# Kernel tuning notes

Hardware: AMD Instinct MI355X
Metric: run time of the kernel (lower is better)

## Reference

```python
import jax, jax.numpy as jnp
import numpy as np

NUM_SITES = 64
PHYS_DIM = 2
BOND_DIM = 32
BATCH = 65536


def _build_mps(num_sites, phys_dim, bond_dim, seed=0):
    """Replicates ImprovedMPS._initialize_tensors + _canonical_form, then
    zero-pads ragged cores into a dense [S, D, p, D] stack."""
    rng = np.random.default_rng(seed)
    tensors = []
    cur = 1
    for i in range(num_sites):
        if i == 0:
            nb = min(bond_dim, phys_dim)
            shape = (1, phys_dim, nb)
            cur = nb
        elif i == num_sites - 1:
            shape = (cur, phys_dim, 1)
        else:
            nb = min(bond_dim, cur * phys_dim)
            shape = (cur, phys_dim, nb)
            cur = nb
        ld, rd = shape[0] * shape[1], shape[2]
        m = (rng.standard_normal((ld, rd)) * 0.1).astype(np.float32)
        if ld >= rd:
            q, _ = np.linalg.qr(m)
            t = q.reshape(shape)
        else:
            q, _ = np.linalg.qr(m.T)
            t = q.T.reshape(shape)
        tensors.append(t.astype(np.float32))
    # left-canonical sweep
    for i in range(num_sites - 1):
        l, p, r = tensors[i].shape
        q, rr = np.linalg.qr(tensors[i].reshape(l * p, r))
        tensors[i] = q.reshape(l, p, q.shape[1]).astype(np.float32)
        nl, npd, nr = tensors[i + 1].shape
        tensors[i + 1] = (rr @ tensors[i + 1].reshape(nl, npd * nr)).reshape(rr.shape[0], npd, nr).astype(np.float32)
    # zero-pad ragged bonds into dense stack [S, D, p, D]
    A = np.zeros((num_sites, bond_dim, phys_dim, bond_dim), dtype=np.float32)
    for i, t in enumerate(tensors):
        l, p, r = t.shape
        A[i, :l, :, :r] = t
    return A


def setup_inputs() -> dict:
    key = jax.random.key(0)
    x_batch = jax.random.normal(key, (BATCH, NUM_SITES, PHYS_DIM), dtype=jnp.float32)
    A = jnp.asarray(_build_mps(NUM_SITES, PHYS_DIM, BOND_DIM))
    return {"x_batch": x_batch, "A": A}


def reference(x_batch, A):
    # x_batch: [B, S, p]; A: [S, D, p, D] (zero-padded ragged MPS cores)
    B = x_batch.shape[0]
    D = A.shape[1]
    # left_vector starts as ones(B,1) in the ragged view == one-hot e0 in padded view
    left0 = jnp.zeros((B, D), dtype=x_batch.dtype).at[:, 0].set(1.0)
    xs = jnp.moveaxis(x_batch, 1, 0)  # [S, B, p]

    def step(left, inp):
        A_i, x_i = inp  # [D, p, D], [B, p]
        # fuses: contracted = einsum('bp,lpd->bld'); left = einsum('bl,bld->bd')
        left = jnp.einsum('bl,bp,lpd->bd', left, x_i, A_i)
        return left, None

    left, _ = jax.lax.scan(step, left0, (A, xs))
    return left[:, :1]  # last core has right bond 1 -> only col 0 is nonzero
```

## Files before the change

### kernel.cpp

```cpp
#include <hip/hip_runtime.h>


typedef _Float16 half8 __attribute__((ext_vector_type(8)));
typedef float floatx16 __attribute__((ext_vector_type(16)));
typedef float f32x4 __attribute__((ext_vector_type(4)));

#define NPAIRS 32
#define CHUNK_ELEMS 16384

__global__ void mps_prep_pair(const float* __restrict__ A, _Float16* __restrict__ Gf) {
    __shared__ float sA0[2048], sA1[2048], sG[4096];
    const int P = blockIdx.x, tid = threadIdx.x;
    const float* a0p = A + (size_t)(2 * P) * 2048;
    const float* a1p = A + (size_t)(2 * P + 1) * 2048;
#pragma unroll
    for (int i = 0; i < 8; ++i) {
        sA0[tid + 256 * i] = a0p[tid + 256 * i];
        sA1[tid + 256 * i] = a1p[tid + 256 * i];
    }
    __syncthreads();
    {
        const int l = tid >> 3, pq = (tid >> 1) & 3, dh16 = (tid & 1) * 16;
        const int p = pq >> 1, q = pq & 1;
        float accv[16];
#pragma unroll
        for (int dd = 0; dd < 16; ++dd) accv[dd] = 0.f;
        for (int m = 0; m < 32; ++m) {
            const float av = sA0[l * 64 + p * 32 + m];
            const float* bp = &sA1[m * 64 + q * 32 + dh16];
#pragma unroll
            for (int dd = 0; dd < 16; ++dd) accv[dd] += av * bp[dd];
        }
#pragma unroll
        for (int dd = 0; dd < 16; ++dd) sG[l * 128 + pq * 32 + dh16 + dd] = accv[dd];
    }
    __syncthreads();
    const int lane = tid & 63;
    const int h    = lane >> 5;
    const int d    = lane & 31;
#pragma unroll
    for (int pass = 0; pass < 2; ++pass) {
        const int kf = (tid >> 6) + pass * 4;
        const int pq = kf >> 1, lh = kf & 1;
        half8 v;
#pragma unroll
        for (int e = 0; e < 8; ++e) {
            const int l = 16 * lh + (e & 3) + 8 * (e >> 2) + 4 * h;
            v[e] = (_Float16)sG[l * 128 + pq * 32 + d];
        }
        reinterpret_cast<half8*>(Gf)[((size_t)P * 8 + kf) * 64 + lane] = v;
    }
}

#define MF32(A_, B_, C_) __builtin_amdgcn_mfma_f32_32x32x16_f16(A_, B_, C_, 0, 0, 0)

#define PAIR1(G, CIN, COUT, XV)                                               \
    {                                                                         \
        half8 FA0_, FA1_;                                                     \
        _Pragma("unroll")                                                     \
        for (int i_ = 0; i_ < 8; ++i_) {                                      \
            FA0_[i_] = (_Float16)CIN[i_];                                     \
            FA1_[i_] = (_Float16)CIN[8 + i_];                                 \
        }                                                                     \
        const _Float16 w0_ = (_Float16)(XV[0] * XV[2]);                       \
        const _Float16 w1_ = (_Float16)(XV[0] * XV[3]);                       \
        const _Float16 w2_ = (_Float16)(XV[1] * XV[2]);                       \
        const _Float16 w3_ = (_Float16)(XV[1] * XV[3]);                       \
        half8 W0_, W1_, W2_, W3_;                                             \
        _Pragma("unroll")                                                     \
        for (int i_ = 0; i_ < 8; ++i_) {                                      \
            W0_[i_] = w0_; W1_[i_] = w1_; W2_[i_] = w2_; W3_[i_] = w3_;       \
        }                                                                     \
        COUT = MF32(G[0], FA0_ * W0_, zv);                                    \
        COUT = MF32(G[1], FA1_ * W0_, COUT);                                  \
        COUT = MF32(G[2], FA0_ * W1_, COUT);                                  \
        COUT = MF32(G[3], FA1_ * W1_, COUT);                                  \
        COUT = MF32(G[4], FA0_ * W2_, COUT);                                  \
        COUT = MF32(G[5], FA1_ * W2_, COUT);                                  \
        COUT = MF32(G[6], FA0_ * W3_, COUT);                                  \
        COUT = MF32(G[7], FA1_ * W3_, COUT);                                  \
    }

#define RD(DST, BUF, PL)                                                      \
    {                                                                         \
        _Pragma("unroll")                                                     \
        for (int f_ = 0; f_ < 8; ++f_)                                        \
            DST[f_] = *(const half8*)&smA[(BUF) * CHUNK_ELEMS                 \
                                          + (((PL) * 8 + f_) * 64 + lane) * 8]; \
    }

#define STAGE(C, BUF)                                                         \
    {                                                                         \
        _Pragma("unroll")                                                     \
        for (int r_ = 0; r_ < 16; ++r_) {                                     \
            const int rec_ = r_ * 2 + wid;                                    \
            const _Float16* g_ = Gf + (size_t)(C) * CHUNK_ELEMS               \
                                 + rec_ * 512 + lane * 8;                     \
            __builtin_amdgcn_global_load_lds(                                 \
                (const __attribute__((address_space(1))) void*)g_,            \
                (__attribute__((address_space(3))) void*)&smA[(BUF) * CHUNK_ELEMS + rec_ * 512], \
                16, 0, 0);                                                    \
        }                                                                     \
    }

#define CHUNKB(C, BUF, XT0, XT1, XN0, XN1)                                    \
    {                                                                         \
        if ((C) < 7) {                                                        \
            STAGE((C) + 1, 1 - (BUF));                                        \
            _Pragma("unroll")                                                 \
            for (int pp_ = 0; pp_ < 4; ++pp_) {                               \
                XN0[pp_] = xp0[4 * ((C) + 1) + pp_];                          \
                XN1[pp_] = xp1[4 * ((C) + 1) + pp_];                          \
            }                                                                 \
        }                                                                     \
        RD(GB, BUF, 1)                                                        \
        PAIR1(GA, c0, d0, XT0[0])                                             \
        PAIR1(GA, c1, d1, XT1[0])                                             \
        RD(GA, BUF, 2)                                                        \
        PAIR1(GB, d0, c0, XT0[1])                                             \
        PAIR1(GB, d1, c1, XT1[1])                                             \
        RD(GB, BUF, 3)                                                        \
        PAIR1(GA, c0, d0, XT0[2])                                             \
        PAIR1(GA, c1, d1, XT1[2])                                             \
        PAIR1(GB, d0, c0, XT0[3])                                             \
        PAIR1(GB, d1, c1, XT1[3])                                             \
        __syncthreads();                                                      \
        if ((C) < 7) RD(GA, 1 - (BUF), 0)                                     \
    }

__global__ __launch_bounds__(128, 1) void mps_main(const float* __restrict__ x,
                                                   const _Float16* __restrict__ Gf,
                                                   float* __restrict__ out) {
    __shared__ __align__(16) _Float16 smA[2 * CHUNK_ELEMS];

    const int lane  = threadIdx.x & 63;
    const int wid   = threadIdx.x >> 6;
    const int wbase = (blockIdx.x * 2 + wid) * 64;
    const int col   = lane & 31;

    const f32x4* xp0 = reinterpret_cast<const f32x4*>(x + (size_t)(wbase + col) * 128);
    const f32x4* xp1 = reinterpret_cast<const f32x4*>(x + (size_t)(wbase + 32 + col) * 128);

    floatx16 zv;
#pragma unroll
    for (int i = 0; i < 16; ++i) zv[i] = 0.f;

    floatx16 c0, c1, d0, d1;
#pragma unroll
    for (int i = 0; i < 16; ++i) { c0[i] = 0.f; c1[i] = 0.f; d0[i] = 0.f; d1[i] = 0.f; }
    if (lane < 32) { c0[0] = 1.f; c1[0] = 1.f; }

    f32x4 xa0[4], xa1[4], xb0[4], xb1[4];
    half8 GA[8], GB[8];

    STAGE(0, 0);
#pragma unroll
    for (int pp = 0; pp < 4; ++pp) { xa0[pp] = xp0[pp]; xa1[pp] = xp1[pp]; }
    __syncthreads();
    RD(GA, 0, 0)

    CHUNKB(0, 0, xa0, xa1, xb0, xb1)
    CHUNKB(1, 1, xb0, xb1, xa0, xa1)
    CHUNKB(2, 0, xa0, xa1, xb0, xb1)
    CHUNKB(3, 1, xb0, xb1, xa0, xa1)
    CHUNKB(4, 0, xa0, xa1, xb0, xb1)
    CHUNKB(5, 1, xb0, xb1, xa0, xa1)
    CHUNKB(6, 0, xa0, xa1, xb0, xb1)
    CHUNKB(7, 1, xb0, xb1, xa0, xa1)

    if (lane < 32) {
        out[wbase + lane]      = c0[0];
        out[wbase + 32 + lane] = c1[0];
    }
}

extern "C" void kernel_launch(void* const* d_in, const int* in_sizes, int n_in,
                              void* d_out, int out_size, void* d_ws, size_t ws_size,
                              hipStream_t stream) {
    const float* x = (const float*)d_in[0];
    const float* A = (const float*)d_in[1];
    float* outp = (float*)d_out;
    _Float16* Gf = (_Float16*)d_ws;

    hipLaunchKernelGGL(mps_prep_pair, dim3(NPAIRS), dim3(256), 0, stream, A, Gf);
    hipLaunchKernelGGL(mps_main, dim3(65536 / 128), dim3(128), 0, stream, x, Gf, outp);
}
```

Before: 29.24 us.

## Split MFMA accumulation chains and stage x through LDS via async loads

Each pair step now keeps two independent MFMA accumulator chains (even and odd K halves) and sums them when forming the next step's input. This halves the length of the dependent MFMA chain. The x inputs are now prefetched into a double-buffered LDS region with global_load_lds alongside the G staging, replacing per-lane register prefetches. This uses more LDS and adds extra adds and LDS reads per step, in exchange for more MFMA instruction-level parallelism and fewer live registers.

```diff
diff --git a/kernel.cpp b/kernel.cpp
--- a/kernel.cpp
+++ b/kernel.cpp
@@ -6,7 +6,8 @@
 typedef float f32x4 __attribute__((ext_vector_type(4)));
 
 #define NPAIRS 32
-#define CHUNK_ELEMS 16384
+#define GCHUNK 16384
+#define XCHUNK 2048
 
 __global__ void mps_prep_pair(const float* __restrict__ A, _Float16* __restrict__ Gf) {
     __shared__ float sA0[2048], sA1[2048], sG[4096];
@@ -54,76 +55,94 @@
 
 #define MF32(A_, B_, C_) __builtin_amdgcn_mfma_f32_32x32x16_f16(A_, B_, C_, 0, 0, 0)
 
-#define PAIR1(G, CIN, COUT, XV)                                               \
+#define PAIRT(G, AA, AB, XQ)                                                  \
     {                                                                         \
         half8 FA0_, FA1_;                                                     \
         _Pragma("unroll")                                                     \
         for (int i_ = 0; i_ < 8; ++i_) {                                      \
-            FA0_[i_] = (_Float16)CIN[i_];                                     \
-            FA1_[i_] = (_Float16)CIN[8 + i_];                                 \
-        }                                                                     \
-        const _Float16 w0_ = (_Float16)(XV[0] * XV[2]);                       \
-        const _Float16 w1_ = (_Float16)(XV[0] * XV[3]);                       \
-        const _Float16 w2_ = (_Float16)(XV[1] * XV[2]);                       \
-        const _Float16 w3_ = (_Float16)(XV[1] * XV[3]);                       \
+            FA0_[i_] = (_Float16)(AA[i_] + AB[i_]);                           \
+            FA1_[i_] = (_Float16)(AA[8 + i_] + AB[8 + i_]);                   \
+        }                                                                     \
+        const _Float16 w0_ = (_Float16)(XQ[0] * XQ[2]);                       \
+        const _Float16 w1_ = (_Float16)(XQ[0] * XQ[3]);                       \
+        const _Float16 w2_ = (_Float16)(XQ[1] * XQ[2]);                       \
+        const _Float16 w3_ = (_Float16)(XQ[1] * XQ[3]);                       \
         half8 W0_, W1_, W2_, W3_;                                             \
         _Pragma("unroll")                                                     \
         for (int i_ = 0; i_ < 8; ++i_) {                                      \
             W0_[i_] = w0_; W1_[i_] = w1_; W2_[i_] = w2_; W3_[i_] = w3_;       \
         }                                                                     \
-        COUT = MF32(G[0], FA0_ * W0_, zv);                                    \
-        COUT = MF32(G[1], FA1_ * W0_, COUT);                                  \
-        COUT = MF32(G[2], FA0_ * W1_, COUT);                                  \
-        COUT = MF32(G[3], FA1_ * W1_, COUT);                                  \
-        COUT = MF32(G[4], FA0_ * W2_, COUT);                                  \
-        COUT = MF32(G[5], FA1_ * W2_, COUT);                                  \
-        COUT = MF32(G[6], FA0_ * W3_, COUT);                                  \
-        COUT = MF32(G[7], FA1_ * W3_, COUT);                                  \
+        AA = MF32(G[0], FA0_ * W0_, zv);                                      \
+        AB = MF32(G[1], FA1_ * W0_, zv);                                      \
+        AA = MF32(G[2], FA0_ * W1_, AA);                                      \
+        AB = MF32(G[3], FA1_ * W1_, AB);                                      \
+        AA = MF32(G[4], FA0_ * W2_, AA);                                      \
+        AB = MF32(G[5], FA1_ * W2_, AB);                                      \
+        AA = MF32(G[6], FA0_ * W3_, AA);                                      \
+        AB = MF32(G[7], FA1_ * W3_, AB);                                      \
     }
 
 #define RD(DST, BUF, PL)                                                      \
     {                                                                         \
         _Pragma("unroll")                                                     \
         for (int f_ = 0; f_ < 8; ++f_)                                        \
-            DST[f_] = *(const half8*)&smA[(BUF) * CHUNK_ELEMS                 \
+            DST[f_] = *(const half8*)&smG[(BUF) * GCHUNK                      \
                                           + (((PL) * 8 + f_) * 64 + lane) * 8]; \
     }
 
-#define STAGE(C, BUF)                                                         \
+#define XRD(BUF, PP, T)                                                       \
+    (*(const f32x4*)&smX[(BUF) * XCHUNK + (PP) * 512 + (wid * 64 + 32 * (T) + col) * 4])
+
+#define STAGEG(C, BUF)                                                        \
     {                                                                         \
         _Pragma("unroll")                                                     \
         for (int r_ = 0; r_ < 16; ++r_) {                                     \
             const int rec_ = r_ * 2 + wid;                                    \
-            const _Float16* g_ = Gf + (size_t)(C) * CHUNK_ELEMS               \
-                                 + rec_ * 512 + lane * 8;                     \
+            const _Float16* g_ = Gf + (size_t)(C) * GCHUNK + rec_ * 512 + lane * 8; \
             __builtin_amdgcn_global_load_lds(                                 \
                 (const __attribute__((address_space(1))) void*)g_,            \
-                (__attribute__((address_space(3))) void*)&smA[(BUF) * CHUNK_ELEMS + rec_ * 512], \
+                (__attribute__((address_space(3))) void*)&smG[(BUF) * GCHUNK + rec_ * 512], \
                 16, 0, 0);                                                    \
         }                                                                     \
     }
 
-#define CHUNKB(C, BUF, XT0, XT1, XN0, XN1)                                    \
-    {                                                                         \
-        if ((C) < 7) {                                                        \
-            STAGE((C) + 1, 1 - (BUF));                                        \
-            _Pragma("unroll")                                                 \
-            for (int pp_ = 0; pp_ < 4; ++pp_) {                               \
-                XN0[pp_] = xp0[4 * ((C) + 1) + pp_];                          \
-                XN1[pp_] = xp1[4 * ((C) + 1) + pp_];                          \
-            }                                                                 \
-        }                                                                     \
+#define STAGEX(C, BUF)                                                        \
+    {                                                                         \
+        _Pragma("unroll")                                                     \
+        for (int r_ = 0; r_ < 4; ++r_) {                                      \
+            const int rec_  = r_ * 2 + wid;                                   \
+            const int quad_ = rec_ >> 1, rowg_ = rec_ & 1;                    \
+            const float* s_ = x + (size_t)(brow + rowg_ * 64 + lane) * 128    \
+                                + 16 * (C) + 4 * quad_;                       \
+            __builtin_amdgcn_global_load_lds(                                 \
+                (const __attribute__((address_space(1))) void*)s_,            \
+                (__attribute__((address_space(3))) void*)&smX[(BUF) * XCHUNK + rec_ * 256], \
+                16, 0, 0);                                                    \
+        }                                                                     \
+    }
+
+#define CHUNKB(C, BUF)                                                        \
+    {                                                                         \
+        if ((C) < 7) { STAGEG((C) + 1, 1 - (BUF)); STAGEX((C) + 1, 1 - (BUF)); } \
         RD(GB, BUF, 1)                                                        \
-        PAIR1(GA, c0, d0, XT0[0])                                             \
-        PAIR1(GA, c1, d1, XT1[0])                                             \
+        {                                                                     \
+            f32x4 xq0_ = XRD(BUF, 0, 0), xq1_ = XRD(BUF, 0, 1);               \
+            PAIRT(GA, aA0, aB0, xq0_) PAIRT(GA, aA1, aB1, xq1_)               \
+        }                                                                     \
         RD(GA, BUF, 2)                                                        \
-        PAIR1(GB, d0, c0, XT0[1])                                             \
-        PAIR1(GB, d1, c1, XT1[1])                                             \
+        {                                                                     \
+            f32x4 xq0_ = XRD(BUF, 1, 0), xq1_ = XRD(BUF, 1, 1);               \
+            PAIRT(GB, aA0, aB0, xq0_) PAIRT(GB, aA1, aB1, xq1_)               \
+        }                                                                     \
         RD(GB, BUF, 3)                                                        \
-        PAIR1(GA, c0, d0, XT0[2])                                             \
-        PAIR1(GA, c1, d1, XT1[2])                                             \
-        PAIR1(GB, d0, c0, XT0[3])                                             \
-        PAIR1(GB, d1, c1, XT1[3])                                             \
+        {                                                                     \
+            f32x4 xq0_ = XRD(BUF, 2, 0), xq1_ = XRD(BUF, 2, 1);               \
+            PAIRT(GA, aA0, aB0, xq0_) PAIRT(GA, aA1, aB1, xq1_)               \
+        }                                                                     \
+        {                                                                     \
+            f32x4 xq0_ = XRD(BUF, 3, 0), xq1_ = XRD(BUF, 3, 1);               \
+            PAIRT(GB, aA0, aB0, xq0_) PAIRT(GB, aA1, aB1, xq1_)               \
+        }                                                                     \
         __syncthreads();                                                      \
         if ((C) < 7) RD(GA, 1 - (BUF), 0)                                     \
     }
@@ -131,46 +150,42 @@
 __global__ __launch_bounds__(128, 1) void mps_main(const float* __restrict__ x,
                                                    const _Float16* __restrict__ Gf,
                                                    float* __restrict__ out) {
-    __shared__ __align__(16) _Float16 smA[2 * CHUNK_ELEMS];
-
-    const int lane  = threadIdx.x & 63;
-    const int wid   = threadIdx.x >> 6;
-    const int wbase = (blockIdx.x * 2 + wid) * 64;
-    const int col   = lane & 31;
-
-    const f32x4* xp0 = reinterpret_cast<const f32x4*>(x + (size_t)(wbase + col) * 128);
-    const f32x4* xp1 = reinterpret_cast<const f32x4*>(x + (size_t)(wbase + 32 + col) * 128);
+    __shared__ __align__(16) _Float16 smG[2 * GCHUNK];
+    __shared__ __align__(16) float    smX[2 * XCHUNK];
+
+    const int lane = threadIdx.x & 63;
+    const int wid  = threadIdx.x >> 6;
+    const int brow = blockIdx.x * 128;
+    const int col  = lane & 31;
 
     floatx16 zv;
 #pragma unroll
     for (int i = 0; i < 16; ++i) zv[i] = 0.f;
 
-    floatx16 c0, c1, d0, d1;
-#pragma unroll
-    for (int i = 0; i < 16; ++i) { c0[i] = 0.f; c1[i] = 0.f; d0[i] = 0.f; d1[i] = 0.f; }
-    if (lane < 32) { c0[0] = 1.f; c1[0] = 1.f; }
-
-    f32x4 xa0[4], xa1[4], xb0[4], xb1[4];
+    floatx16 aA0, aB0, aA1, aB1;
+#pragma unroll
+    for (int i = 0; i < 16; ++i) { aA0[i] = 0.f; aB0[i] = 0.f; aA1[i] = 0.f; aB1[i] = 0.f; }
+    if (lane < 32) { aA0[0] = 1.f; aA1[0] = 1.f; }
+
     half8 GA[8], GB[8];
 
-    STAGE(0, 0);
-#pragma unroll
-    for (int pp = 0; pp < 4; ++pp) { xa0[pp] = xp0[pp]; xa1[pp] = xp1[pp]; }
+    STAGEG(0, 0);
+    STAGEX(0, 0);
     __syncthreads();
     RD(GA, 0, 0)
 
-    CHUNKB(0, 0, xa0, xa1, xb0, xb1)
-    CHUNKB(1, 1, xb0, xb1, xa0, xa1)
-    CHUNKB(2, 0, xa0, xa1, xb0, xb1)
-    CHUNKB(3, 1, xb0, xb1, xa0, xa1)
-    CHUNKB(4, 0, xa0, xa1, xb0, xb1)
-    CHUNKB(5, 1, xb0, xb1, xa0, xa1)
-    CHUNKB(6, 0, xa0, xa1, xb0, xb1)
-    CHUNKB(7, 1, xb0, xb1, xa0, xa1)
+    CHUNKB(0, 0)
+    CHUNKB(1, 1)
+    CHUNKB(2, 0)
+    CHUNKB(3, 1)
+    CHUNKB(4, 0)
+    CHUNKB(5, 1)
+    CHUNKB(6, 0)
+    CHUNKB(7, 1)
 
     if (lane < 32) {
-        out[wbase + lane]      = c0[0];
-        out[wbase + 32 + lane] = c1[0];
+        out[brow + wid * 64 + lane]      = aA0[0] + aB0[0];
+        out[brow + wid * 64 + 32 + lane] = aA1[0] + aB1[0];
     }
 }
 
```

Result: slower. 44.68 us (+52.8%).

## Restructure MPS main kernel to 4 waves per block with one chain each

Applied to the files above, without the earlier changes.

Each wave now carries a single 32-sample chain instead of two interleaved chains, and blocks grow to 256 threads with two blocks per CU. The x inputs for the block are preloaded once into LDS as fp16 in a transposed, padded layout, so the per-step global x loads go away. G chunks are staged at a smaller granularity, one site-pair per half-chunk, over 16 chunks. This trades the per-wave ILP of two independent MFMA chains for more waves resident per CU, and reads G from LDS right before each use instead of double-buffering it in registers. The x weights are also now formed in fp16 rather than fp32, which may cost some precision.

```diff
diff --git a/kernel.cpp b/kernel.cpp
--- a/kernel.cpp
+++ b/kernel.cpp
@@ -2,11 +2,13 @@
 
 
 typedef _Float16 half8 __attribute__((ext_vector_type(8)));
+typedef _Float16 half4 __attribute__((ext_vector_type(4)));
 typedef float floatx16 __attribute__((ext_vector_type(16)));
 typedef float f32x4 __attribute__((ext_vector_type(4)));
 
 #define NPAIRS 32
-#define CHUNK_ELEMS 16384
+#define GCH 8192
+#define XSTRIDE 129
 
 __global__ void mps_prep_pair(const float* __restrict__ A, _Float16* __restrict__ Gf) {
     __shared__ float sA0[2048], sA1[2048], sG[4096];
@@ -54,124 +56,99 @@
 
 #define MF32(A_, B_, C_) __builtin_amdgcn_mfma_f32_32x32x16_f16(A_, B_, C_, 0, 0, 0)
 
-#define PAIR1(G, CIN, COUT, XV)                                               \
-    {                                                                         \
-        half8 FA0_, FA1_;                                                     \
-        _Pragma("unroll")                                                     \
-        for (int i_ = 0; i_ < 8; ++i_) {                                      \
-            FA0_[i_] = (_Float16)CIN[i_];                                     \
-            FA1_[i_] = (_Float16)CIN[8 + i_];                                 \
-        }                                                                     \
-        const _Float16 w0_ = (_Float16)(XV[0] * XV[2]);                       \
-        const _Float16 w1_ = (_Float16)(XV[0] * XV[3]);                       \
-        const _Float16 w2_ = (_Float16)(XV[1] * XV[2]);                       \
-        const _Float16 w3_ = (_Float16)(XV[1] * XV[3]);                       \
-        half8 W0_, W1_, W2_, W3_;                                             \
-        _Pragma("unroll")                                                     \
-        for (int i_ = 0; i_ < 8; ++i_) {                                      \
-            W0_[i_] = w0_; W1_[i_] = w1_; W2_[i_] = w2_; W3_[i_] = w3_;       \
-        }                                                                     \
-        COUT = MF32(G[0], FA0_ * W0_, zv);                                    \
-        COUT = MF32(G[1], FA1_ * W0_, COUT);                                  \
-        COUT = MF32(G[2], FA0_ * W1_, COUT);                                  \
-        COUT = MF32(G[3], FA1_ * W1_, COUT);                                  \
-        COUT = MF32(G[4], FA0_ * W2_, COUT);                                  \
-        COUT = MF32(G[5], FA1_ * W2_, COUT);                                  \
-        COUT = MF32(G[6], FA0_ * W3_, COUT);                                  \
-        COUT = MF32(G[7], FA1_ * W3_, COUT);                                  \
-    }
-
-#define RD(DST, BUF, PL)                                                      \
+#define STAGEG(C, BUF)                                                        \
     {                                                                         \
         _Pragma("unroll")                                                     \
-        for (int f_ = 0; f_ < 8; ++f_)                                        \
-            DST[f_] = *(const half8*)&smA[(BUF) * CHUNK_ELEMS                 \
-                                          + (((PL) * 8 + f_) * 64 + lane) * 8]; \
-    }
-
-#define STAGE(C, BUF)                                                         \
-    {                                                                         \
-        _Pragma("unroll")                                                     \
-        for (int r_ = 0; r_ < 16; ++r_) {                                     \
-            const int rec_ = r_ * 2 + wid;                                    \
-            const _Float16* g_ = Gf + (size_t)(C) * CHUNK_ELEMS               \
-                                 + rec_ * 512 + lane * 8;                     \
+        for (int r_ = 0; r_ < 4; ++r_) {                                      \
+            const int rec_ = r_ * 4 + wid;                                    \
+            const _Float16* g_ = Gf + (size_t)(C) * GCH + rec_ * 512 + lane * 8; \
             __builtin_amdgcn_global_load_lds(                                 \
                 (const __attribute__((address_space(1))) void*)g_,            \
-                (__attribute__((address_space(3))) void*)&smA[(BUF) * CHUNK_ELEMS + rec_ * 512], \
+                (__attribute__((address_space(3))) void*)&smG[(BUF) * GCH + rec_ * 512], \
                 16, 0, 0);                                                    \
         }                                                                     \
     }
 
-#define CHUNKB(C, BUF, XT0, XT1, XN0, XN1)                                    \
+#define PAIRDO(BUF, LP, P)                                                    \
     {                                                                         \
-        if ((C) < 7) {                                                        \
-            STAGE((C) + 1, 1 - (BUF));                                        \
-            _Pragma("unroll")                                                 \
-            for (int pp_ = 0; pp_ < 4; ++pp_) {                               \
-                XN0[pp_] = xp0[4 * ((C) + 1) + pp_];                          \
-                XN1[pp_] = xp1[4 * ((C) + 1) + pp_];                          \
-            }                                                                 \
+        const half4 xq_ = smX[(P) * XSTRIDE + r];                             \
+        const _Float16 w00_ = xq_[0] * xq_[2];                                \
+        const _Float16 w01_ = xq_[0] * xq_[3];                                \
+        const _Float16 w10_ = xq_[1] * xq_[2];                                \
+        const _Float16 w11_ = xq_[1] * xq_[3];                                \
+        half8 G_[8];                                                          \
+        _Pragma("unroll")                                                     \
+        for (int f_ = 0; f_ < 8; ++f_)                                        \
+            G_[f_] = *(const half8*)&smG[(BUF) * GCH + (((LP) * 8 + f_) * 64 + lane) * 8]; \
+        half8 FA0_, FA1_;                                                     \
+        _Pragma("unroll")                                                     \
+        for (int i_ = 0; i_ < 8; ++i_) {                                      \
+            FA0_[i_] = (_Float16)acc[i_];                                     \
+            FA1_[i_] = (_Float16)acc[8 + i_];                                 \
         }                                                                     \
-        RD(GB, BUF, 1)                                                        \
-        PAIR1(GA, c0, d0, XT0[0])                                             \
-        PAIR1(GA, c1, d1, XT1[0])                                             \
-        RD(GA, BUF, 2)                                                        \
-        PAIR1(GB, d0, c0, XT0[1])                                             \
-        PAIR1(GB, d1, c1, XT1[1])                                             \
-        RD(GB, BUF, 3)                                                        \
-        PAIR1(GA, c0, d0, XT0[2])                                             \
-        PAIR1(GA, c1, d1, XT1[2])                                             \
-        PAIR1(GB, d0, c0, XT0[3])                                             \
-        PAIR1(GB, d1, c1, XT1[3])                                             \
-        __syncthreads();                                                      \
-        if ((C) < 7) RD(GA, 1 - (BUF), 0)                                     \
+        floatx16 t_;                                                          \
+        t_ = MF32(G_[0], FA0_ * w00_, zv);                                    \
+        t_ = MF32(G_[1], FA1_ * w00_, t_);                                    \
+        t_ = MF32(G_[2], FA0_ * w01_, t_);                                    \
+        t_ = MF32(G_[3], FA1_ * w01_, t_);                                    \
+        t_ = MF32(G_[4], FA0_ * w10_, t_);                                    \
+        t_ = MF32(G_[5], FA1_ * w10_, t_);                                    \
+        t_ = MF32(G_[6], FA0_ * w11_, t_);                                    \
+        t_ = MF32(G_[7], FA1_ * w11_, t_);                                    \
+        acc = t_;                                                             \
     }
 
-__global__ __launch_bounds__(128, 1) void mps_main(const float* __restrict__ x,
+#define CHUNK(C, BUF)                                                         \
+    {                                                                         \
+        if ((C) < 15) STAGEG((C) + 1, 1 - (BUF));                             \
+        PAIRDO(BUF, 0, 2 * (C))                                               \
+        PAIRDO(BUF, 1, 2 * (C) + 1)                                           \
+        __syncthreads();                                                      \
+    }
+
+__global__ __launch_bounds__(256, 2) void mps_main(const float* __restrict__ x,
                                                    const _Float16* __restrict__ Gf,
                                                    float* __restrict__ out) {
-    __shared__ __align__(16) _Float16 smA[2 * CHUNK_ELEMS];
+    __shared__ __align__(16) _Float16 smG[2 * GCH];
+    __shared__ __align__(8)  half4    smX[32 * XSTRIDE];
 
-    const int lane  = threadIdx.x & 63;
-    const int wid   = threadIdx.x >> 6;
-    const int wbase = (blockIdx.x * 2 + wid) * 64;
-    const int col   = lane & 31;
+    const int tid  = threadIdx.x;
+    const int lane = tid & 63;
+    const int wid  = tid >> 6;
+    const int brow = blockIdx.x * 128;
+    const int col  = lane & 31;
+    const int r    = wid * 32 + col;
 
-    const f32x4* xp0 = reinterpret_cast<const f32x4*>(x + (size_t)(wbase + col) * 128);
-    const f32x4* xp1 = reinterpret_cast<const f32x4*>(x + (size_t)(wbase + 32 + col) * 128);
+    STAGEG(0, 0);
+
+#pragma unroll
+    for (int i = 0; i < 16; ++i) {
+        const int j   = i * 256 + tid;
+        const int row = j >> 5, q = j & 31;
+        const f32x4 v = *(const f32x4*)(x + (size_t)(brow + row) * 128 + 4 * q);
+        half4 hv;
+        hv[0] = (_Float16)v[0]; hv[1] = (_Float16)v[1];
+        hv[2] = (_Float16)v[2]; hv[3] = (_Float16)v[3];
+        smX[q * XSTRIDE + row] = hv;
+    }
 
     floatx16 zv;
 #pragma unroll
     for (int i = 0; i < 16; ++i) zv[i] = 0.f;
 
-    floatx16 c0, c1, d0, d1;
+    floatx16 acc;
 #pragma unroll
-    for (int i = 0; i < 16; ++i) { c0[i] = 0.f; c1[i] = 0.f; d0[i] = 0.f; d1[i] = 0.f; }
-    if (lane < 32) { c0[0] = 1.f; c1[0] = 1.f; }
+    for (int i = 0; i < 16; ++i) acc[i] = 0.f;
+    if (lane < 32) acc[0] = 1.f;
 
-    f32x4 xa0[4], xa1[4], xb0[4], xb1[4];
-    half8 GA[8], GB[8];
+    __syncthreads();
 
-    STAGE(0, 0);
-#pragma unroll
-    for (int pp = 0; pp < 4; ++pp) { xa0[pp] = xp0[pp]; xa1[pp] = xp1[pp]; }
-    __syncthreads();
-    RD(GA, 0, 0)
+    CHUNK(0, 0)   CHUNK(1, 1)   CHUNK(2, 0)   CHUNK(3, 1)
+    CHUNK(4, 0)   CHUNK(5, 1)   CHUNK(6, 0)   CHUNK(7, 1)
+    CHUNK(8, 0)   CHUNK(9, 1)   CHUNK(10, 0)  CHUNK(11, 1)
+    CHUNK(12, 0)  CHUNK(13, 1)  CHUNK(14, 0)  CHUNK(15, 1)
 
-    CHUNKB(0, 0, xa0, xa1, xb0, xb1)
-    CHUNKB(1, 1, xb0, xb1, xa0, xa1)
-    CHUNKB(2, 0, xa0, xa1, xb0, xb1)
-    CHUNKB(3, 1, xb0, xb1, xa0, xa1)
-    CHUNKB(4, 0, xa0, xa1, xb0, xb1)
-    CHUNKB(5, 1, xb0, xb1, xa0, xa1)
-    CHUNKB(6, 0, xa0, xa1, xb0, xb1)
-    CHUNKB(7, 1, xb0, xb1, xa0, xa1)
-
-    if (lane < 32) {
-        out[wbase + lane]      = c0[0];
-        out[wbase + 32 + lane] = c1[0];
-    }
+    if (lane < 32) out[brow + wid * 32 + lane] = acc[0];
 }
 
 extern "C" void kernel_launch(void* const* d_in, const int* in_sizes, int n_in,
@@ -183,5 +160,5 @@
     _Float16* Gf = (_Float16*)d_ws;
 
     hipLaunchKernelGGL(mps_prep_pair, dim3(NPAIRS), dim3(256), 0, stream, A, Gf);
-    hipLaunchKernelGGL(mps_main, dim3(65536 / 128), dim3(128), 0, stream, x, Gf, outp);
+    hipLaunchKernelGGL(mps_main, dim3(65536 / 128), dim3(256), 0, stream, x, Gf, outp);
 }
```

New measurement: 28.77 us. About the same (-1.6%).
